# Optimization experiments

Hardware: AMD Instinct MI355X
Metric: run time of the kernel (lower is better)

Reference implementation:

```python
import jax, jax.numpy as jnp
import numpy as np

N = 50000      # nodes
E = 1_600_000  # edges
IN, H, H2, OUT = 256, 128, 64, 2
EPS = 1e-5     # BatchNorm eps


def setup_inputs() -> dict:
    key = jax.random.key(0)
    ks = jax.random.split(key, 18)
    inp = {
        "x": jax.random.normal(ks[0], (N, IN), dtype=jnp.float32),
        "edge_index": jax.random.randint(ks[1], (2, E), 0, N, dtype=jnp.int64),
        # GCNConv 1
        "W1": jax.random.normal(ks[2], (IN, H), dtype=jnp.float32) / np.sqrt(IN),
        "b1": jnp.zeros((H,), dtype=jnp.float32),
        "g1": jnp.ones((H,), dtype=jnp.float32),
        "be1": jnp.zeros((H,), dtype=jnp.float32),
        "m1": jax.random.normal(ks[3], (H,), dtype=jnp.float32) * 0.1,
        "v1": jax.random.uniform(ks[4], (H,), dtype=jnp.float32, minval=0.5, maxval=1.5),
        # GCNConv 2
        "W2": jax.random.normal(ks[5], (H, H2), dtype=jnp.float32) / np.sqrt(H),
        "b2": jnp.zeros((H2,), dtype=jnp.float32),
        "g2": jnp.ones((H2,), dtype=jnp.float32),
        "be2": jnp.zeros((H2,), dtype=jnp.float32),
        "m2": jax.random.normal(ks[6], (H2,), dtype=jnp.float32) * 0.1,
        "v2": jax.random.uniform(ks[7], (H2,), dtype=jnp.float32, minval=0.5, maxval=1.5),
        # final linear
        "Wl": jax.random.normal(ks[8], (H2, OUT), dtype=jnp.float32) / np.sqrt(H2),
        "bl": jnp.zeros((OUT,), dtype=jnp.float32),
    }
    return inp


def _gcn_conv(x, W, b, src, dst, n_nodes):
    # PyG GCNConv: linear transform, then symmetric-normalized aggregation
    # with self-loops (gcn_norm, improved=False, fill_value=1).
    xw = x @ W                                            # [N, H]
    ones = jnp.ones((src.shape[0],), dtype=x.dtype)
    deg = jax.ops.segment_sum(ones, dst, num_segments=n_nodes) + 1.0  # +1 self-loop
    dinv = jax.lax.rsqrt(deg)                             # deg^{-1/2}
    norm = dinv[src] * dinv[dst]                          # [E]
    msgs = xw[src] * norm[:, None]                        # [E, H] gather
    agg = jax.ops.segment_sum(msgs, dst, num_segments=n_nodes)  # scatter-add
    agg = agg + xw * (1.0 / deg)[:, None]                 # self-loop term
    return agg + b


def _bn_relu(x, gamma, beta, mean, var):
    # inference-mode BatchNorm1d + ReLU
    xhat = (x - mean) * jax.lax.rsqrt(var + EPS)
    return jax.nn.relu(xhat * gamma + beta)


def reference(x, edge_index, W1, b1, g1, be1, m1, v1,
              W2, b2, g2, be2, m2, v2, Wl, bl):
    src, dst = edge_index[0], edge_index[1]
    h = _gcn_conv(x, W1, b1, src, dst, N)
    h = _bn_relu(h, g1, be1, m1, v1)
    # dropout is identity in eval mode
    h = _gcn_conv(h, W2, b2, src, dst, N)
    h = _bn_relu(h, g2, be2, m2, v2)
    return h @ Wl + bl
```

## Files before the change

### kernel.cpp

```cpp
#include <hip/hip_runtime.h>

#define N_NODES 50000
#define N_EDGES 1600000
#define IN_F 256
#define H1_F 128
#define H2_F 64
#define OUT_F 2
#define BN_EPS 1e-5f

#define NBUK 782
#define BCAP 3584
#define CHUNK 8192
#define NCHUNK 196

typedef __attribute__((ext_vector_type(8))) short bf16x8;
typedef __attribute__((ext_vector_type(4))) float f32x4;
typedef __attribute__((ext_vector_type(4))) int   i32x4;
typedef __attribute__((ext_vector_type(4))) unsigned u32x4;

__device__ __forceinline__ unsigned short f2b(float f) {
    union { float f; unsigned u; } v; v.f = f;
    unsigned r = (v.u + 0x7FFFu + ((v.u >> 16) & 1u)) >> 16;
    return (unsigned short)r;
}
__device__ __forceinline__ float b2f(unsigned short b) {
    union { unsigned u; float f; } v; v.u = ((unsigned)b) << 16;
    return v.f;
}
__device__ __forceinline__ void add2(float& a0, float& a1, unsigned u) {
    union { unsigned u; float f; } lo, hi;
    lo.u = u << 16;
    hi.u = u & 0xFFFF0000u;
    a0 += lo.f; a1 += hi.f;
}

__launch_bounds__(512)
__global__ void chist_kernel(const int* __restrict__ dst, int* __restrict__ h,
                             int* __restrict__ tot) {
    __shared__ int lh[NBUK];
    const int c = blockIdx.x;
    for (int i = threadIdx.x; i < NBUK; i += 512) lh[i] = 0;
    __syncthreads();
    const int e0 = c * CHUNK;
    const int e1 = min(e0 + CHUNK, N_EDGES);
    const i32x4* p = (const i32x4*)(dst + e0);
    const int n4 = (e1 - e0) >> 2;
    for (int i = threadIdx.x; i < n4; i += 512) {
        i32x4 d = __builtin_nontemporal_load(p + i);
        atomicAdd(&lh[d.x >> 6], 1);
        atomicAdd(&lh[d.y >> 6], 1);
        atomicAdd(&lh[d.z >> 6], 1);
        atomicAdd(&lh[d.w >> 6], 1);
    }
    __syncthreads();
    for (int i = threadIdx.x; i < NBUK; i += 512) {
        int v = lh[i];
        h[(size_t)i * NCHUNK + c] = v;
        if (v) atomicAdd(&tot[i], v);
    }
}

__global__ void bscan_kernel(const int* __restrict__ tot, int* __restrict__ boff,
                             int* __restrict__ rowptr) {
    __shared__ int tmp[1024];
    const int t = threadIdx.x;
    int v = (t < NBUK) ? tot[t] : 0;
    tmp[t] = v;
    __syncthreads();
    for (int off = 1; off < 1024; off <<= 1) {
        int a = (t >= off) ? tmp[t - off] : 0;
        __syncthreads();
        tmp[t] += a;
        __syncthreads();
    }
    if (t < NBUK) boff[t] = tmp[t] - v;
    if (t == 0) { boff[NBUK] = N_EDGES; rowptr[N_NODES] = N_EDGES; }
}

__global__ void boffs_kernel(int* __restrict__ h, const int* __restrict__ boff) {
    const int t = blockIdx.x * blockDim.x + threadIdx.x;
    if (t >= NBUK) return;
    int run = boff[t];
    int* row = h + (size_t)t * NCHUNK;
    for (int c = 0; c < NCHUNK; ++c) {
        int v = row[c];
        row[c] = run;
        run += v;
    }
}

__launch_bounds__(512)
__global__ void cscatter_kernel(const int* __restrict__ src, const int* __restrict__ dst,
                                const int* __restrict__ h, unsigned* __restrict__ bedges) {
    __shared__ int cur[NBUK];
    const int c = blockIdx.x;
    for (int i = threadIdx.x; i < NBUK; i += 512) cur[i] = h[(size_t)i * NCHUNK + c];
    __syncthreads();
    const int e0 = c * CHUNK;
    const int e1 = min(e0 + CHUNK, N_EDGES);
    const i32x4* pd = (const i32x4*)(dst + e0);
    const i32x4* ps = (const i32x4*)(src + e0);
    const int n4 = (e1 - e0) >> 2;
    for (int i = threadIdx.x; i < n4; i += 512) {
        i32x4 d = __builtin_nontemporal_load(pd + i);
        i32x4 s = __builtin_nontemporal_load(ps + i);
        int slot;
        slot = atomicAdd(&cur[d.x >> 6], 1); bedges[slot] = (unsigned)s.x | ((unsigned)d.x << 16);
        slot = atomicAdd(&cur[d.y >> 6], 1); bedges[slot] = (unsigned)s.y | ((unsigned)d.y << 16);
        slot = atomicAdd(&cur[d.z >> 6], 1); bedges[slot] = (unsigned)s.z | ((unsigned)d.z << 16);
        slot = atomicAdd(&cur[d.w >> 6], 1); bedges[slot] = (unsigned)s.w | ((unsigned)d.w << 16);
    }
}

__launch_bounds__(256)
__global__ void build_kernel(const unsigned* __restrict__ bedges, const int* __restrict__ boff,
                             unsigned short* __restrict__ perm, int* __restrict__ rowptr,
                             float* __restrict__ dinv) {
    __shared__ unsigned e_lds[BCAP];
    __shared__ unsigned short p_lds[BCAP];
    __shared__ int ncnt[64], ncur[64];

    const int b = blockIdx.x;
    const int t = threadIdx.x;
    const int start = boff[b];
    const int end   = boff[b + 1];
    const int cnt   = end - start;
    const bool fits = (cnt <= BCAP);

    if (t < 64) ncnt[t] = 0;
    __syncthreads();

    for (int i = t; i < cnt; i += 256) {
        unsigned e = bedges[start + i];
        if (fits) e_lds[i] = e;
        atomicAdd(&ncnt[(e >> 16) & 63], 1);
    }
    __syncthreads();

    if (t == 0) {
        int a = 0;
        for (int i = 0; i < 64; ++i) { ncur[i] = a; a += ncnt[i]; }
    }
    __syncthreads();

    if (t < 64) {
        int node = b * 64 + t;
        if (node < N_NODES) {
            rowptr[node] = start + ncur[t];
            dinv[node]   = rsqrtf((float)ncnt[t] + 1.0f);
        }
    }
    __syncthreads();

    for (int i = t; i < cnt; i += 256) {
        unsigned e = fits ? e_lds[i] : bedges[start + i];
        int slot = atomicAdd(&ncur[(e >> 16) & 63], 1);
        unsigned short s = (unsigned short)(e & 0xFFFFu);
        if (fits) p_lds[slot] = s;
        else      perm[start + slot] = s;
    }
    if (fits) {
        __syncthreads();
        for (int i = t; i < cnt; i += 256) perm[start + i] = p_lds[i];
    }
}

__global__ void wt_kernel(const float* __restrict__ W, unsigned short* __restrict__ WT,
                          int K, int N) {
    int i = blockIdx.x * blockDim.x + threadIdx.x;
    if (i < N * K) {
        int n = i / K, k = i % K;
        WT[i] = f2b(W[(size_t)k * N + n]);
    }
}

__global__ void bnprep_kernel(const float* __restrict__ g, const float* __restrict__ be,
                              const float* __restrict__ m, const float* __restrict__ v,
                              const float* __restrict__ bias, float* __restrict__ sc,
                              float* __restrict__ sh, int F) {
    int f = blockIdx.x * blockDim.x + threadIdx.x;
    if (f < F) {
        float s = g[f] * rsqrtf(v[f] + BN_EPS);
        sc[f] = s;
        sh[f] = (bias[f] - m[f]) * s + be[f];
    }
}

template <int KSTEPS, int NTILES, bool A_BF16>
__launch_bounds__(256)
__global__ void mfma_gemm_kernel(const void* __restrict__ Ap, const unsigned short* __restrict__ BT,
                                 const float* __restrict__ dscale, unsigned short* __restrict__ C,
                                 int M) {
    constexpr int K  = KSTEPS * 32;
    constexpr int NF = NTILES * 16;
    const int wave = threadIdx.x >> 6;
    const int lane = threadIdx.x & 63;
    const int r0   = (blockIdx.x * 4 + wave) * 16;
    const int m    = lane & 15;
    const int kb   = lane >> 4;

    int arow = r0 + m;
    if (arow >= M) arow = M - 1;

    f32x4 acc[NTILES];
#pragma unroll
    for (int nt = 0; nt < NTILES; ++nt) acc[nt] = (f32x4)(0.f);

#pragma unroll
    for (int ks = 0; ks < KSTEPS; ++ks) {
        const int k0 = ks * 32 + kb * 8;
        bf16x8 a;
        if constexpr (A_BF16) {
            a = *(const bf16x8*)((const unsigned short*)Ap + (size_t)arow * K + k0);
        } else {
            const float* af = (const float*)Ap + (size_t)arow * K + k0;
            f32x4 lo = __builtin_nontemporal_load((const f32x4*)af);
            f32x4 hi = __builtin_nontemporal_load((const f32x4*)(af + 4));
            union { bf16x8 v; unsigned short u[8]; } pk;
            pk.u[0] = f2b(lo.x); pk.u[1] = f2b(lo.y); pk.u[2] = f2b(lo.z); pk.u[3] = f2b(lo.w);
            pk.u[4] = f2b(hi.x); pk.u[5] = f2b(hi.y); pk.u[6] = f2b(hi.z); pk.u[7] = f2b(hi.w);
            a = pk.v;
        }
#pragma unroll
        for (int nt = 0; nt < NTILES; ++nt) {
            bf16x8 b = *(const bf16x8*)(BT + (size_t)(nt * 16 + m) * K + k0);
            acc[nt] = __builtin_amdgcn_mfma_f32_16x16x32_bf16(a, b, acc[nt], 0, 0, 0);
        }
    }

#pragma unroll
    for (int reg = 0; reg < 4; ++reg) {
        const int r = r0 + kb * 4 + reg;
        if (r < M) {
            const float ds = dscale[r];
#pragma unroll
            for (int nt = 0; nt < NTILES; ++nt)
                C[(size_t)r * NF + nt * 16 + m] = f2b(acc[nt][reg] * ds);
        }
    }
}

template <int HF, bool FINAL>
__launch_bounds__(256)
__global__ void agg_kernel(const int* __restrict__ rowptr, const unsigned short* __restrict__ perm,
                           const unsigned short* __restrict__ xw, const float* __restrict__ dinv,
                           const float* __restrict__ sc, const float* __restrict__ sh,
                           const float* __restrict__ Wl, const float* __restrict__ bl,
                           void* __restrict__ outp) {
    constexpr int LPE = HF / 8;
    constexpr int G   = 64 / LPE;
    const int wave = threadIdx.x >> 6;
    const int node = blockIdx.x * 4 + wave;
    if (node >= N_NODES) return;
    const int lane = threadIdx.x & 63;
    const int grp  = lane / LPE;
    const int fl   = (lane % LPE) * 8;

    float aA[8], aB[8];
#pragma unroll
    for (int i = 0; i < 8; ++i) { aA[i] = 0.f; aB[i] = 0.f; }

    if (grp == 0) {
        u32x4 u = *(const u32x4*)(xw + (size_t)node * HF + fl);
#pragma unroll
        for (int i = 0; i < 4; ++i) add2(aA[2 * i], aA[2 * i + 1], u[i]);
    }

    const int start = rowptr[node];
    const int end   = rowptr[node + 1];
    for (int base = start; base < end; base += 64) {
        int pidx = base + lane;
        int pv = (int)__builtin_nontemporal_load(perm + (pidx < end ? pidx : end - 1));
        int ne = end - base;
        if (ne > 64) ne = 64;
        if (ne == 64) {
#pragma unroll
            for (int j = 0; j < 64; j += 2 * G) {
                int s0 = __shfl(pv, j + grp);
                int s1 = __shfl(pv, j + G + grp);
                u32x4 u0 = *(const u32x4*)(xw + (size_t)s0 * HF + fl);
                u32x4 u1 = *(const u32x4*)(xw + (size_t)s1 * HF + fl);
#pragma unroll
                for (int i = 0; i < 4; ++i) add2(aA[2 * i], aA[2 * i + 1], u0[i]);
#pragma unroll
                for (int i = 0; i < 4; ++i) add2(aB[2 * i], aB[2 * i + 1], u1[i]);
            }
        } else {
            for (int j = 0; j < ne; j += G) {
                int s = __shfl(pv, j + grp);
                if (j + grp < ne) {
                    u32x4 u = *(const u32x4*)(xw + (size_t)s * HF + fl);
#pragma unroll
                    for (int i = 0; i < 4; ++i) add2(aA[2 * i], aA[2 * i + 1], u[i]);
                }
            }
        }
    }

#pragma unroll
    for (int i = 0; i < 8; ++i) aA[i] += aB[i];

#pragma unroll
    for (int off = LPE; off < 64; off <<= 1)
#pragma unroll
        for (int i = 0; i < 8; ++i) aA[i] += __shfl_xor(aA[i], off);

    const float dv = dinv[node];
    f32x4 scl = *(const f32x4*)(sc + fl);
    f32x4 sch = *(const f32x4*)(sc + fl + 4);
    f32x4 shl = *(const f32x4*)(sh + fl);
    f32x4 shh = *(const f32x4*)(sh + fl + 4);
    float y[8];
#pragma unroll
    for (int i = 0; i < 4; ++i) {
        y[i]     = fmaxf(aA[i] * (dv * scl[i]) + shl[i], 0.f);
        y[i + 4] = fmaxf(aA[i + 4] * (dv * sch[i]) + shh[i], 0.f);
    }

    if constexpr (!FINAL) {
        if (lane < LPE) {
            u32x4 o;
#pragma unroll
            for (int i = 0; i < 4; ++i)
                o[i] = (unsigned)f2b(y[2 * i]) | ((unsigned)f2b(y[2 * i + 1]) << 16);
            __builtin_nontemporal_store(o, (u32x4*)((unsigned short*)outp + (size_t)node * HF + fl));
        }
    } else {
        float p0 = 0.f, p1 = 0.f;
#pragma unroll
        for (int i = 0; i < 8; ++i) {
            float w0 = Wl[(fl + i) * 2 + 0];
            float w1 = Wl[(fl + i) * 2 + 1];
            p0 += y[i] * w0;
            p1 += y[i] * w1;
        }
#pragma unroll
        for (int off = 1; off < LPE; off <<= 1) {
            p0 += __shfl_xor(p0, off);
            p1 += __shfl_xor(p1, off);
        }
        if (lane == 0) {
            float* o = (float*)outp;
            o[(size_t)node * 2 + 0] = p0 + bl[0];
            o[(size_t)node * 2 + 1] = p1 + bl[1];
        }
    }
}

extern "C" void kernel_launch(void* const* d_in, const int* in_sizes, int n_in,
                              void* d_out, int out_size, void* d_ws, size_t ws_size,
                              hipStream_t stream) {
    const float* x   = (const float*)d_in[0];
    const int*   ei  = (const int*)d_in[1];
    const float* W1  = (const float*)d_in[2];
    const float* b1  = (const float*)d_in[3];
    const float* g1  = (const float*)d_in[4];
    const float* be1 = (const float*)d_in[5];
    const float* m1  = (const float*)d_in[6];
    const float* v1  = (const float*)d_in[7];
    const float* W2  = (const float*)d_in[8];
    const float* b2  = (const float*)d_in[9];
    const float* g2  = (const float*)d_in[10];
    const float* be2 = (const float*)d_in[11];
    const float* m2  = (const float*)d_in[12];
    const float* v2  = (const float*)d_in[13];
    const float* Wl  = (const float*)d_in[14];
    const float* bl  = (const float*)d_in[15];

    const int* src = ei;
    const int* dst = ei + N_EDGES;

    int*            h      = (int*)d_ws;
    int*            tot    = h + NBUK * NCHUNK;
    int*            boff   = tot + 1024;
    int*            rowptr = boff + 1024;
    float*          dinv   = (float*)(rowptr + 50016);
    float*          sc1    = dinv + 50016;
    float*          sh1    = sc1 + 128;
    float*          sc2    = sh1 + 128;
    float*          sh2    = sc2 + 64;
    unsigned*       bedges = (unsigned*)(sh2 + 64);
    unsigned short* perm   = (unsigned short*)(bedges + N_EDGES);
    unsigned short* xwb    = perm + N_EDGES;
    unsigned short* h1b    = xwb + (size_t)N_NODES * H1_F;
    unsigned short* w1t    = h1b + (size_t)N_NODES * H1_F;
    unsigned short* w2t    = w1t + H1_F * IN_F;

    hipMemsetAsync(tot, 0, 1024 * sizeof(int), stream);

    chist_kernel<<<NCHUNK, 512, 0, stream>>>(dst, h, tot);
    bscan_kernel<<<1, 1024, 0, stream>>>(tot, boff, rowptr);
    boffs_kernel<<<(NBUK + 255) / 256, 256, 0, stream>>>(h, boff);
    cscatter_kernel<<<NCHUNK, 512, 0, stream>>>(src, dst, h, bedges);
    build_kernel<<<NBUK, 256, 0, stream>>>(bedges, boff, perm, rowptr, dinv);

    wt_kernel<<<(H1_F * IN_F + 255) / 256, 256, 0, stream>>>(W1, w1t, IN_F, H1_F);
    wt_kernel<<<(H2_F * H1_F + 255) / 256, 256, 0, stream>>>(W2, w2t, H1_F, H2_F);
    bnprep_kernel<<<1, 128, 0, stream>>>(g1, be1, m1, v1, b1, sc1, sh1, H1_F);
    bnprep_kernel<<<1, 64, 0, stream>>>(g2, be2, m2, v2, b2, sc2, sh2, H2_F);

    mfma_gemm_kernel<IN_F / 32, H1_F / 16, false><<<(N_NODES + 63) / 64, 256, 0, stream>>>(
        x, w1t, dinv, xwb, N_NODES);
    agg_kernel<H1_F, false><<<(N_NODES + 3) / 4, 256, 0, stream>>>(
        rowptr, perm, xwb, dinv, sc1, sh1, nullptr, nullptr, h1b);

    mfma_gemm_kernel<H1_F / 32, H2_F / 16, true><<<(N_NODES + 63) / 64, 256, 0, stream>>>(
        h1b, w2t, dinv, xwb, N_NODES);
    agg_kernel<H2_F, true><<<(N_NODES + 3) / 4, 256, 0, stream>>>(
        rowptr, perm, xwb, dinv, sc2, sh2, Wl, bl, (float*)d_out);
}
```

Before: 275.8 us.

## Use smaller edge chunks, wave-parallel offset scan, single accumulator in aggregation

Edge chunks for the counting-sort histogram and scatter shrink from 8192 to 2048 edges with 256-thread blocks, giving 782 blocks instead of 196 to fill the GPU better. The per-bucket offset scan now uses one wave per bucket with shuffle-based prefix sums rather than one serial thread per bucket, since the histogram matrix is four times larger. The aggregation kernel drops its second accumulator array to cut register pressure, at the cost of less memory-level parallelism per iteration. The per-bucket histogram workspace grows fourfold.

```diff
diff --git a/kernel.cpp b/kernel.cpp
--- a/kernel.cpp
+++ b/kernel.cpp
@@ -10,8 +10,8 @@
 
 #define NBUK 782
 #define BCAP 3584
-#define CHUNK 8192
-#define NCHUNK 196
+#define CHUNK 2048
+#define NCHUNK 782
 
 typedef __attribute__((ext_vector_type(8))) short bf16x8;
 typedef __attribute__((ext_vector_type(4))) float f32x4;
@@ -34,18 +34,18 @@
     a0 += lo.f; a1 += hi.f;
 }
 
-__launch_bounds__(512)
+__launch_bounds__(256)
 __global__ void chist_kernel(const int* __restrict__ dst, int* __restrict__ h,
                              int* __restrict__ tot) {
     __shared__ int lh[NBUK];
     const int c = blockIdx.x;
-    for (int i = threadIdx.x; i < NBUK; i += 512) lh[i] = 0;
+    for (int i = threadIdx.x; i < NBUK; i += 256) lh[i] = 0;
     __syncthreads();
     const int e0 = c * CHUNK;
     const int e1 = min(e0 + CHUNK, N_EDGES);
     const i32x4* p = (const i32x4*)(dst + e0);
     const int n4 = (e1 - e0) >> 2;
-    for (int i = threadIdx.x; i < n4; i += 512) {
+    for (int i = threadIdx.x; i < n4; i += 256) {
         i32x4 d = __builtin_nontemporal_load(p + i);
         atomicAdd(&lh[d.x >> 6], 1);
         atomicAdd(&lh[d.y >> 6], 1);
@@ -53,7 +53,7 @@
         atomicAdd(&lh[d.w >> 6], 1);
     }
     __syncthreads();
-    for (int i = threadIdx.x; i < NBUK; i += 512) {
+    for (int i = threadIdx.x; i < NBUK; i += 256) {
         int v = lh[i];
         h[(size_t)i * NCHUNK + c] = v;
         if (v) atomicAdd(&tot[i], v);
@@ -77,31 +77,40 @@
     if (t == 0) { boff[NBUK] = N_EDGES; rowptr[N_NODES] = N_EDGES; }
 }
 
+__launch_bounds__(256)
 __global__ void boffs_kernel(int* __restrict__ h, const int* __restrict__ boff) {
-    const int t = blockIdx.x * blockDim.x + threadIdx.x;
-    if (t >= NBUK) return;
-    int run = boff[t];
-    int* row = h + (size_t)t * NCHUNK;
-    for (int c = 0; c < NCHUNK; ++c) {
-        int v = row[c];
-        row[c] = run;
-        run += v;
-    }
-}
-
-__launch_bounds__(512)
+    const int b = (blockIdx.x * blockDim.x + threadIdx.x) >> 6;
+    if (b >= NBUK) return;
+    const int lane = threadIdx.x & 63;
+    int run = boff[b];
+    int* row = h + (size_t)b * NCHUNK;
+    for (int c0 = 0; c0 < NCHUNK; c0 += 64) {
+        int idx = c0 + lane;
+        int v = (idx < NCHUNK) ? row[idx] : 0;
+        int s = v;
+#pragma unroll
+        for (int off = 1; off < 64; off <<= 1) {
+            int t = __shfl_up(s, off);
+            if (lane >= off) s += t;
+        }
+        if (idx < NCHUNK) row[idx] = run + (s - v);
+        run += __shfl(s, 63);
+    }
+}
+
+__launch_bounds__(256)
 __global__ void cscatter_kernel(const int* __restrict__ src, const int* __restrict__ dst,
                                 const int* __restrict__ h, unsigned* __restrict__ bedges) {
     __shared__ int cur[NBUK];
     const int c = blockIdx.x;
-    for (int i = threadIdx.x; i < NBUK; i += 512) cur[i] = h[(size_t)i * NCHUNK + c];
+    for (int i = threadIdx.x; i < NBUK; i += 256) cur[i] = h[(size_t)i * NCHUNK + c];
     __syncthreads();
     const int e0 = c * CHUNK;
     const int e1 = min(e0 + CHUNK, N_EDGES);
     const i32x4* pd = (const i32x4*)(dst + e0);
     const i32x4* ps = (const i32x4*)(src + e0);
     const int n4 = (e1 - e0) >> 2;
-    for (int i = threadIdx.x; i < n4; i += 512) {
+    for (int i = threadIdx.x; i < n4; i += 256) {
         i32x4 d = __builtin_nontemporal_load(pd + i);
         i32x4 s = __builtin_nontemporal_load(ps + i);
         int slot;
@@ -256,9 +265,9 @@
     const int grp  = lane / LPE;
     const int fl   = (lane % LPE) * 8;
 
-    float aA[8], aB[8];
-#pragma unroll
-    for (int i = 0; i < 8; ++i) { aA[i] = 0.f; aB[i] = 0.f; }
+    float aA[8];
+#pragma unroll
+    for (int i = 0; i < 8; ++i) aA[i] = 0.f;
 
     if (grp == 0) {
         u32x4 u = *(const u32x4*)(xw + (size_t)node * HF + fl);
@@ -275,15 +284,11 @@
         if (ne > 64) ne = 64;
         if (ne == 64) {
 #pragma unroll
-            for (int j = 0; j < 64; j += 2 * G) {
-                int s0 = __shfl(pv, j + grp);
-                int s1 = __shfl(pv, j + G + grp);
-                u32x4 u0 = *(const u32x4*)(xw + (size_t)s0 * HF + fl);
-                u32x4 u1 = *(const u32x4*)(xw + (size_t)s1 * HF + fl);
-#pragma unroll
-                for (int i = 0; i < 4; ++i) add2(aA[2 * i], aA[2 * i + 1], u0[i]);
-#pragma unroll
-                for (int i = 0; i < 4; ++i) add2(aB[2 * i], aB[2 * i + 1], u1[i]);
+            for (int j = 0; j < 64; j += G) {
+                int s = __shfl(pv, j + grp);
+                u32x4 u = *(const u32x4*)(xw + (size_t)s * HF + fl);
+#pragma unroll
+                for (int i = 0; i < 4; ++i) add2(aA[2 * i], aA[2 * i + 1], u[i]);
             }
         } else {
             for (int j = 0; j < ne; j += G) {
@@ -298,9 +303,6 @@
     }
 
 #pragma unroll
-    for (int i = 0; i < 8; ++i) aA[i] += aB[i];
-
-#pragma unroll
     for (int off = LPE; off < 64; off <<= 1)
 #pragma unroll
         for (int i = 0; i < 8; ++i) aA[i] += __shfl_xor(aA[i], off);
@@ -329,10 +331,8 @@
         float p0 = 0.f, p1 = 0.f;
 #pragma unroll
         for (int i = 0; i < 8; ++i) {
-            float w0 = Wl[(fl + i) * 2 + 0];
-            float w1 = Wl[(fl + i) * 2 + 1];
-            p0 += y[i] * w0;
-            p1 += y[i] * w1;
+            p0 += y[i] * Wl[(fl + i) * 2 + 0];
+            p1 += y[i] * Wl[(fl + i) * 2 + 1];
         }
 #pragma unroll
         for (int off = 1; off < LPE; off <<= 1) {
@@ -371,7 +371,7 @@
     const int* dst = ei + N_EDGES;
 
     int*            h      = (int*)d_ws;
-    int*            tot    = h + NBUK * NCHUNK;
+    int*            tot    = h + (size_t)NBUK * NCHUNK;
     int*            boff   = tot + 1024;
     int*            rowptr = boff + 1024;
     float*          dinv   = (float*)(rowptr + 50016);
@@ -388,10 +388,10 @@
 
     hipMemsetAsync(tot, 0, 1024 * sizeof(int), stream);
 
-    chist_kernel<<<NCHUNK, 512, 0, stream>>>(dst, h, tot);
+    chist_kernel<<<NCHUNK, 256, 0, stream>>>(dst, h, tot);
     bscan_kernel<<<1, 1024, 0, stream>>>(tot, boff, rowptr);
-    boffs_kernel<<<(NBUK + 255) / 256, 256, 0, stream>>>(h, boff);
-    cscatter_kernel<<<NCHUNK, 512, 0, stream>>>(src, dst, h, bedges);
+    boffs_kernel<<<(NBUK * 64 + 255) / 256, 256, 0, stream>>>(h, boff);
+    cscatter_kernel<<<NCHUNK, 256, 0, stream>>>(src, dst, h, bedges);
     build_kernel<<<NBUK, 256, 0, stream>>>(bedges, boff, perm, rowptr, dinv);
 
     wt_kernel<<<(H1_F * IN_F + 255) / 256, 256, 0, stream>>>(W1, w1t, IN_F, H1_F);
```

After: 270.3 us. 1.02x faster.
